# Kernel tuning notes

Hardware: AMD Instinct MI355X
Metric: run time of the kernel (lower is better)

The kernel has to match this reference:

```python
import jax, jax.numpy as jnp
import numpy as np

SCALE = 10.0
THRESH = 1e-3   # nn.Threshold(eps, 0)
NORM_EPS = 1e-12  # F.normalize default eps
LEAKY_SLOPE = 0.01


def _proj(x, W1, W2):
    # x: [B, C, L]; conv1x1 == channel matmul
    h = jnp.einsum('oc,bcl->bol', W1, x)
    h = jnp.where(h >= 0, h, LEAKY_SLOPE * h)
    return jnp.einsum('oc,bcl->bol', W2, h)


def _l2norm(x):
    # normalize over channel dim (dim=1), torch F.normalize semantics
    n = jnp.sqrt(jnp.sum(x * x, axis=1, keepdims=True))
    return x / jnp.maximum(n, NORM_EPS)


def setup_inputs() -> dict:
    key = jax.random.key(0)
    k1, k2, k3, k4 = jax.random.split(key, 4)
    B, C, L, OUT = 4, 64, 4096, 64
    query = jax.random.normal(k1, (B, C, L), dtype=jnp.float32)
    kv = jax.random.normal(k2, (B, C, L), dtype=jnp.float32)
    W1 = jax.random.normal(k3, (2 * C, C), dtype=jnp.float32) * (1.0 / np.sqrt(C))
    W2 = jax.random.normal(k4, (OUT, 2 * C), dtype=jnp.float32) * (1.0 / np.sqrt(2 * C))
    return {"query": query, "key": kv, "W1": W1, "W2": W2}


def reference(query, key, W1, W2):
    # self_attention=True: query_conv is key_conv (shared weights)
    q = _l2norm(_proj(query, W1, W2))   # [B, O, L]
    k = _l2norm(_proj(key, W1, W2))     # [B, O, L]
    scores = jnp.einsum('bcl,bcm->blm', q, k) * SCALE  # [B, L, L]
    w = jax.nn.softmax(scores, axis=-1)
    return jnp.where(w > THRESH, w, 0.0)
```

## Files before the change

### kernel.cpp

```cpp
#include <hip/hip_runtime.h>
#include <math.h>

#define B 4
#define C 64
#define L 4096
#define OUTC 64
#define SCALE 10.0f
#define THRESH 1e-3f

typedef float v4f __attribute__((ext_vector_type(4)));
typedef short bf16x8 __attribute__((ext_vector_type(8)));
typedef unsigned short us8 __attribute__((ext_vector_type(8)));

__device__ __forceinline__ unsigned short f2bf(float x) {
    unsigned int u = __float_as_uint(x);
    u += 0x7fffu + ((u >> 16) & 1u);
    return (unsigned short)(u >> 16);
}
__device__ __forceinline__ float bf2f(unsigned short h) {
    return __uint_as_float(((unsigned int)h) << 16);
}
__device__ __forceinline__ v4f mfma16(bf16x8 a, bf16x8 b, v4f c) {
    return __builtin_amdgcn_mfma_f32_16x16x32_bf16(a, b, c, 0, 0, 0);
}

__global__ void __launch_bounds__(256) proj_kernel(
    const float* __restrict__ q_in, const float* __restrict__ k_in,
    const float* __restrict__ W1, const float* __restrict__ W2,
    unsigned short* __restrict__ Qh, unsigned short* __restrict__ Ql,
    unsigned short* __restrict__ Kh, unsigned short* __restrict__ Kl)
{
    int bid   = blockIdx.x;
    int which = bid >> 8;
    int b     = (bid >> 6) & 3;
    int l0    = (bid & 63) << 6;
    int t     = threadIdx.x;
    int g     = t >> 6;
    int l     = t & 63;

    const float* __restrict__ src =
        (which ? k_in : q_in) + (size_t)b * C * L + l0 + l;
    unsigned short* __restrict__ dh = which ? Kh : Qh;
    unsigned short* __restrict__ dl = which ? Kl : Ql;

    __shared__ float Ht[128][65];
    __shared__ float red[4][64];

    float xr[C];
    #pragma unroll
    for (int c = 0; c < C; ++c)
        xr[c] = src[(size_t)c * L];

    #pragma unroll 1
    for (int oo = 0; oo < 32; oo += 4) {
        #pragma unroll
        for (int u = 0; u < 4; ++u) {
            int o = g * 32 + oo + u;
            float h0 = 0.f, h1 = 0.f, h2 = 0.f, h3 = 0.f;
            #pragma unroll
            for (int c = 0; c < C; c += 4) {
                h0 = fmaf(W1[o * C + c + 0], xr[c + 0], h0);
                h1 = fmaf(W1[o * C + c + 1], xr[c + 1], h1);
                h2 = fmaf(W1[o * C + c + 2], xr[c + 2], h2);
                h3 = fmaf(W1[o * C + c + 3], xr[c + 3], h3);
            }
            float h = (h0 + h1) + (h2 + h3);
            Ht[o][l] = (h >= 0.0f) ? h : 0.01f * h;
        }
    }
    __syncthreads();

    float y[16];
    #pragma unroll
    for (int u = 0; u < 16; ++u) y[u] = 0.f;

    #pragma unroll 1
    for (int hh = 0; hh < 2 * C; hh += 16) {
        float hr[16];
        #pragma unroll
        for (int r = 0; r < 16; ++r)
            hr[r] = Ht[hh + r][l];
        #pragma unroll
        for (int u = 0; u < 16; ++u) {
            int o = g * 16 + u;
            #pragma unroll
            for (int h = 0; h < 16; ++h)
                y[u] = fmaf(W2[o * (2 * C) + hh + h], hr[h], y[u]);
        }
    }

    float ss = 0.f;
    #pragma unroll
    for (int u = 0; u < 16; ++u) ss = fmaf(y[u], y[u], ss);
    red[g][l] = ss;
    __syncthreads();
    float tot = red[0][l] + red[1][l] + red[2][l] + red[3][l];
    float inv = 1.0f / fmaxf(sqrtf(tot), 1e-12f);

    unsigned short hs[16], ls[16];
    #pragma unroll
    for (int u = 0; u < 16; ++u) {
        float val = y[u] * inv;
        hs[u] = f2bf(val);
        ls[u] = f2bf(val - bf2f(hs[u]));
    }
    size_t rowoff = ((size_t)b * L + l0 + l) * 64 + (size_t)g * 16;
    *(us8*)(dh + rowoff)     = *(us8*)&hs[0];
    *(us8*)(dh + rowoff + 8) = *(us8*)&hs[8];
    *(us8*)(dl + rowoff)     = *(us8*)&ls[0];
    *(us8*)(dl + rowoff + 8) = *(us8*)&ls[8];
}

__global__ void __launch_bounds__(512) scores_kernel(
    const unsigned short* __restrict__ Qh, const unsigned short* __restrict__ Ql,
    const unsigned short* __restrict__ Kh, const unsigned short* __restrict__ Kl,
    float* __restrict__ out)
{
    int bid  = blockIdx.x;
    int b    = bid >> 6;
    int r0   = (bid & 63) << 6;
    int t    = threadIdx.x;
    int wave = t >> 6;
    int lane = t & 63;
    int quad = lane >> 4;
    int ln   = lane & 15;

    bf16x8 aQ[4][2][2];
    {
        size_t qbase = ((size_t)b * L + r0) * 64;
        #pragma unroll
        for (int rt = 0; rt < 4; ++rt) {
            size_t rowb = qbase + (size_t)(rt * 16 + ln) * 64 + quad * 8;
            #pragma unroll
            for (int c0 = 0; c0 < 2; ++c0) {
                aQ[rt][c0][0] = *(const bf16x8*)(Qh + rowb + c0 * 32);
                aQ[rt][c0][1] = *(const bf16x8*)(Ql + rowb + c0 * 32);
            }
        }
    }

    const size_t kbase = (size_t)b * L * 64;
    __shared__ float wsum[64][8];
    __shared__ float rinv[64];

    v4f ps[4];
    #pragma unroll
    for (int rt = 0; rt < 4; ++rt) ps[rt] = (v4f){0.f, 0.f, 0.f, 0.f};

    #pragma unroll 1
    for (int ct = 0; ct < 32; ++ct) {
        int m0 = wave * 512 + ct * 16;
        size_t kr = kbase + (size_t)(m0 + ln) * 64 + quad * 8;
        bf16x8 bh0 = *(const bf16x8*)(Kh + kr);
        bf16x8 bl0 = *(const bf16x8*)(Kl + kr);
        bf16x8 bh1 = *(const bf16x8*)(Kh + kr + 32);
        bf16x8 bl1 = *(const bf16x8*)(Kl + kr + 32);
        #pragma unroll
        for (int rt = 0; rt < 4; ++rt) {
            v4f acc = (v4f){0.f, 0.f, 0.f, 0.f};
            acc = mfma16(aQ[rt][0][0], bh0, acc);
            acc = mfma16(aQ[rt][0][1], bh0, acc);
            acc = mfma16(aQ[rt][0][0], bl0, acc);
            acc = mfma16(aQ[rt][1][0], bh1, acc);
            acc = mfma16(aQ[rt][1][1], bh1, acc);
            acc = mfma16(aQ[rt][1][0], bl1, acc);
            #pragma unroll
            for (int r = 0; r < 4; ++r)
                ps[rt][r] += __expf(fmaf(SCALE, acc[r], -SCALE));
        }
    }

    #pragma unroll
    for (int rt = 0; rt < 4; ++rt) {
        #pragma unroll
        for (int r = 0; r < 4; ++r) {
            float s = ps[rt][r];
            s += __shfl_xor(s, 1);
            s += __shfl_xor(s, 2);
            s += __shfl_xor(s, 4);
            s += __shfl_xor(s, 8);
            if (ln == 0) wsum[rt * 16 + quad * 4 + r][wave] = s;
        }
    }
    __syncthreads();
    if (t < 64) {
        float s = 0.f;
        #pragma unroll
        for (int w = 0; w < 8; ++w) s += wsum[t][w];
        rinv[t] = 1.0f / s;
    }
    __syncthreads();

    float rv[4][4];
    #pragma unroll
    for (int rt = 0; rt < 4; ++rt)
        #pragma unroll
        for (int r = 0; r < 4; ++r)
            rv[rt][r] = rinv[rt * 16 + quad * 4 + r];

    float* __restrict__ outb = out + ((size_t)b * L + r0) * L;
    #pragma unroll 1
    for (int ct = 0; ct < 32; ++ct) {
        int m0 = wave * 512 + ct * 16;
        size_t kr = kbase + (size_t)(m0 + ln) * 64 + quad * 8;
        bf16x8 bh0 = *(const bf16x8*)(Kh + kr);
        bf16x8 bl0 = *(const bf16x8*)(Kl + kr);
        bf16x8 bh1 = *(const bf16x8*)(Kh + kr + 32);
        bf16x8 bl1 = *(const bf16x8*)(Kl + kr + 32);
        #pragma unroll
        for (int rt = 0; rt < 4; ++rt) {
            v4f acc = (v4f){0.f, 0.f, 0.f, 0.f};
            acc = mfma16(aQ[rt][0][0], bh0, acc);
            acc = mfma16(aQ[rt][0][1], bh0, acc);
            acc = mfma16(aQ[rt][0][0], bl0, acc);
            acc = mfma16(aQ[rt][1][0], bh1, acc);
            acc = mfma16(aQ[rt][1][1], bh1, acc);
            acc = mfma16(aQ[rt][1][0], bl1, acc);
            #pragma unroll
            for (int r = 0; r < 4; ++r) {
                float w = __expf(fmaf(SCALE, acc[r], -SCALE)) * rv[rt][r];
                w = (w > THRESH) ? w : 0.f;
                outb[(size_t)(rt * 16 + quad * 4 + r) * L + m0 + ln] = w;
            }
        }
    }
}

extern "C" void kernel_launch(void* const* d_in, const int* in_sizes, int n_in,
                              void* d_out, int out_size, void* d_ws, size_t ws_size,
                              hipStream_t stream) {
    const float* query = (const float*)d_in[0];
    const float* key   = (const float*)d_in[1];
    const float* W1    = (const float*)d_in[2];
    const float* W2    = (const float*)d_in[3];
    float* out = (float*)d_out;

    unsigned short* Qh = (unsigned short*)d_ws;
    unsigned short* Ql = Qh + (size_t)B * L * OUTC;
    unsigned short* Kh = Ql + (size_t)B * L * OUTC;
    unsigned short* Kl = Kh + (size_t)B * L * OUTC;

    hipLaunchKernelGGL(proj_kernel, dim3(512), dim3(256), 0, stream,
                       query, key, W1, W2, Qh, Ql, Kh, Kl);
    hipLaunchKernelGGL(scores_kernel, dim3(256), dim3(512), 0, stream,
                       Qh, Ql, Kh, Kl, out);
}
```

Measured before the change: 436.5 us.

## Halve query rows per block, prefetch K tiles, and use nontemporal output stores

The scores kernel now handles 32 query rows per block instead of 64, doubling the grid to 512 blocks so more of the GPU's compute units have work. It declares a minimum of 4 blocks per multiprocessor in the launch bounds. Both K passes load the next K tile into registers one iteration ahead, and the 256 MB probability output is written with nontemporal stores to reduce cache pollution. Each block still reads all of K twice, so total K traffic per output row doubles, and the occupancy hint may push the compiler into register spills.

```diff
diff --git a/kernel.cpp b/kernel.cpp
--- a/kernel.cpp
+++ b/kernel.cpp
@@ -111,25 +111,25 @@
     *(us8*)(dl + rowoff + 8) = *(us8*)&ls[8];
 }
 
-__global__ void __launch_bounds__(512) scores_kernel(
+__global__ void __launch_bounds__(512, 4) scores_kernel(
     const unsigned short* __restrict__ Qh, const unsigned short* __restrict__ Ql,
     const unsigned short* __restrict__ Kh, const unsigned short* __restrict__ Kl,
     float* __restrict__ out)
 {
     int bid  = blockIdx.x;
-    int b    = bid >> 6;
-    int r0   = (bid & 63) << 6;
+    int b    = bid >> 7;
+    int r0   = (bid & 127) << 5;
     int t    = threadIdx.x;
     int wave = t >> 6;
     int lane = t & 63;
     int quad = lane >> 4;
     int ln   = lane & 15;
 
-    bf16x8 aQ[4][2][2];
+    bf16x8 aQ[2][2][2];
     {
         size_t qbase = ((size_t)b * L + r0) * 64;
         #pragma unroll
-        for (int rt = 0; rt < 4; ++rt) {
+        for (int rt = 0; rt < 2; ++rt) {
             size_t rowb = qbase + (size_t)(rt * 16 + ln) * 64 + quad * 8;
             #pragma unroll
             for (int c0 = 0; c0 < 2; ++c0) {
@@ -140,38 +140,48 @@
     }
 
     const size_t kbase = (size_t)b * L * 64;
-    __shared__ float wsum[64][8];
-    __shared__ float rinv[64];
-
-    v4f ps[4];
-    #pragma unroll
-    for (int rt = 0; rt < 4; ++rt) ps[rt] = (v4f){0.f, 0.f, 0.f, 0.f};
-
-    #pragma unroll 1
-    for (int ct = 0; ct < 32; ++ct) {
-        int m0 = wave * 512 + ct * 16;
-        size_t kr = kbase + (size_t)(m0 + ln) * 64 + quad * 8;
-        bf16x8 bh0 = *(const bf16x8*)(Kh + kr);
-        bf16x8 bl0 = *(const bf16x8*)(Kl + kr);
-        bf16x8 bh1 = *(const bf16x8*)(Kh + kr + 32);
-        bf16x8 bl1 = *(const bf16x8*)(Kl + kr + 32);
-        #pragma unroll
-        for (int rt = 0; rt < 4; ++rt) {
-            v4f acc = (v4f){0.f, 0.f, 0.f, 0.f};
-            acc = mfma16(aQ[rt][0][0], bh0, acc);
-            acc = mfma16(aQ[rt][0][1], bh0, acc);
-            acc = mfma16(aQ[rt][0][0], bl0, acc);
-            acc = mfma16(aQ[rt][1][0], bh1, acc);
-            acc = mfma16(aQ[rt][1][1], bh1, acc);
-            acc = mfma16(aQ[rt][1][0], bl1, acc);
-            #pragma unroll
-            for (int r = 0; r < 4; ++r)
-                ps[rt][r] += __expf(fmaf(SCALE, acc[r], -SCALE));
-        }
-    }
-
-    #pragma unroll
-    for (int rt = 0; rt < 4; ++rt) {
+    __shared__ float wsum[32][8];
+    __shared__ float rinv[32];
+
+    v4f ps[2];
+    ps[0] = (v4f){0.f, 0.f, 0.f, 0.f};
+    ps[1] = (v4f){0.f, 0.f, 0.f, 0.f};
+
+    {
+        size_t kr0 = kbase + (size_t)(wave * 512 + ln) * 64 + quad * 8;
+        bf16x8 bh0 = *(const bf16x8*)(Kh + kr0);
+        bf16x8 bl0 = *(const bf16x8*)(Kl + kr0);
+        bf16x8 bh1 = *(const bf16x8*)(Kh + kr0 + 32);
+        bf16x8 bl1 = *(const bf16x8*)(Kl + kr0 + 32);
+
+        #pragma unroll 1
+        for (int ct = 0; ct < 32; ++ct) {
+            int ctn = (ct + 1) & 31;
+            size_t krn = kbase + (size_t)(wave * 512 + ctn * 16 + ln) * 64 + quad * 8;
+            bf16x8 nh0 = *(const bf16x8*)(Kh + krn);
+            bf16x8 nl0 = *(const bf16x8*)(Kl + krn);
+            bf16x8 nh1 = *(const bf16x8*)(Kh + krn + 32);
+            bf16x8 nl1 = *(const bf16x8*)(Kl + krn + 32);
+
+            #pragma unroll
+            for (int rt = 0; rt < 2; ++rt) {
+                v4f acc = (v4f){0.f, 0.f, 0.f, 0.f};
+                acc = mfma16(aQ[rt][0][0], bh0, acc);
+                acc = mfma16(aQ[rt][0][1], bh0, acc);
+                acc = mfma16(aQ[rt][0][0], bl0, acc);
+                acc = mfma16(aQ[rt][1][0], bh1, acc);
+                acc = mfma16(aQ[rt][1][1], bh1, acc);
+                acc = mfma16(aQ[rt][1][0], bl1, acc);
+                #pragma unroll
+                for (int r = 0; r < 4; ++r)
+                    ps[rt][r] += __expf(fmaf(SCALE, acc[r], -SCALE));
+            }
+            bh0 = nh0; bl0 = nl0; bh1 = nh1; bl1 = nl1;
+        }
+    }
+
+    #pragma unroll
+    for (int rt = 0; rt < 2; ++rt) {
         #pragma unroll
         for (int r = 0; r < 4; ++r) {
             float s = ps[rt][r];
@@ -183,7 +193,7 @@
         }
     }
     __syncthreads();
-    if (t < 64) {
+    if (t < 32) {
         float s = 0.f;
         #pragma unroll
         for (int w = 0; w < 8; ++w) s += wsum[t][w];
@@ -191,37 +201,49 @@
     }
     __syncthreads();
 
-    float rv[4][4];
-    #pragma unroll
-    for (int rt = 0; rt < 4; ++rt)
+    float rv[2][4];
+    #pragma unroll
+    for (int rt = 0; rt < 2; ++rt)
         #pragma unroll
         for (int r = 0; r < 4; ++r)
             rv[rt][r] = rinv[rt * 16 + quad * 4 + r];
 
     float* __restrict__ outb = out + ((size_t)b * L + r0) * L;
-    #pragma unroll 1
-    for (int ct = 0; ct < 32; ++ct) {
-        int m0 = wave * 512 + ct * 16;
-        size_t kr = kbase + (size_t)(m0 + ln) * 64 + quad * 8;
-        bf16x8 bh0 = *(const bf16x8*)(Kh + kr);
-        bf16x8 bl0 = *(const bf16x8*)(Kl + kr);
-        bf16x8 bh1 = *(const bf16x8*)(Kh + kr + 32);
-        bf16x8 bl1 = *(const bf16x8*)(Kl + kr + 32);
-        #pragma unroll
-        for (int rt = 0; rt < 4; ++rt) {
-            v4f acc = (v4f){0.f, 0.f, 0.f, 0.f};
-            acc = mfma16(aQ[rt][0][0], bh0, acc);
-            acc = mfma16(aQ[rt][0][1], bh0, acc);
-            acc = mfma16(aQ[rt][0][0], bl0, acc);
-            acc = mfma16(aQ[rt][1][0], bh1, acc);
-            acc = mfma16(aQ[rt][1][1], bh1, acc);
-            acc = mfma16(aQ[rt][1][0], bl1, acc);
-            #pragma unroll
-            for (int r = 0; r < 4; ++r) {
-                float w = __expf(fmaf(SCALE, acc[r], -SCALE)) * rv[rt][r];
-                w = (w > THRESH) ? w : 0.f;
-                outb[(size_t)(rt * 16 + quad * 4 + r) * L + m0 + ln] = w;
-            }
+    {
+        size_t kr0 = kbase + (size_t)(wave * 512 + ln) * 64 + quad * 8;
+        bf16x8 bh0 = *(const bf16x8*)(Kh + kr0);
+        bf16x8 bl0 = *(const bf16x8*)(Kl + kr0);
+        bf16x8 bh1 = *(const bf16x8*)(Kh + kr0 + 32);
+        bf16x8 bl1 = *(const bf16x8*)(Kl + kr0 + 32);
+
+        #pragma unroll 1
+        for (int ct = 0; ct < 32; ++ct) {
+            int m0  = wave * 512 + ct * 16;
+            int ctn = (ct + 1) & 31;
+            size_t krn = kbase + (size_t)(wave * 512 + ctn * 16 + ln) * 64 + quad * 8;
+            bf16x8 nh0 = *(const bf16x8*)(Kh + krn);
+            bf16x8 nl0 = *(const bf16x8*)(Kl + krn);
+            bf16x8 nh1 = *(const bf16x8*)(Kh + krn + 32);
+            bf16x8 nl1 = *(const bf16x8*)(Kl + krn + 32);
+
+            #pragma unroll
+            for (int rt = 0; rt < 2; ++rt) {
+                v4f acc = (v4f){0.f, 0.f, 0.f, 0.f};
+                acc = mfma16(aQ[rt][0][0], bh0, acc);
+                acc = mfma16(aQ[rt][0][1], bh0, acc);
+                acc = mfma16(aQ[rt][0][0], bl0, acc);
+                acc = mfma16(aQ[rt][1][0], bh1, acc);
+                acc = mfma16(aQ[rt][1][1], bh1, acc);
+                acc = mfma16(aQ[rt][1][0], bl1, acc);
+                #pragma unroll
+                for (int r = 0; r < 4; ++r) {
+                    float w = __expf(fmaf(SCALE, acc[r], -SCALE)) * rv[rt][r];
+                    w = (w > THRESH) ? w : 0.f;
+                    __builtin_nontemporal_store(
+                        w, outb + (size_t)(rt * 16 + quad * 4 + r) * L + m0 + ln);
+                }
+            }
+            bh0 = nh0; bl0 = nl0; bh1 = nh1; bl1 = nl1;
         }
     }
 }
@@ -242,6 +264,6 @@
 
     hipLaunchKernelGGL(proj_kernel, dim3(512), dim3(256), 0, stream,
                        query, key, W1, W2, Qh, Ql, Kh, Kl);
-    hipLaunchKernelGGL(scores_kernel, dim3(256), dim3(512), 0, stream,
+    hipLaunchKernelGGL(scores_kernel, dim3(512), dim3(512), 0, stream,
                        Qh, Ql, Kh, Kl, out);
 }
```

Result: no change. 435.8 us (-0.1%).
